# Kernel optimization log

Hardware: AMD Instinct MI355X
Metric: run time of the kernel (lower is better)

Reference implementation:

```python
import jax, jax.numpy as jnp
import numpy as np

NC = 80            # num_classes
REG_MAX = 16
STRIDES = (8, 16, 32)
IMG = 640.0
TOPK = 10
TAL_ALPHA = 0.5
TAL_BETA = 6.0
L_BOX, L_CLS, L_DFL = 7.5, 0.5, 1.5
EPS = 1e-9
NEG = -1e8


def bbox_iou(b1, b2, ciou=False, eps=1e-7):
    # b1, b2: (..., 4) xyxy, broadcastable
    inter_wh = jnp.clip(jnp.minimum(b1[..., 2:], b2[..., 2:]) - jnp.maximum(b1[..., :2], b2[..., :2]), 0.0)
    inter = inter_wh[..., 0] * inter_wh[..., 1]
    w1 = jnp.clip(b1[..., 2] - b1[..., 0], 0.0); h1 = jnp.clip(b1[..., 3] - b1[..., 1], 0.0)
    w2 = jnp.clip(b2[..., 2] - b2[..., 0], 0.0); h2 = jnp.clip(b2[..., 3] - b2[..., 1], 0.0)
    union = w1 * h1 + w2 * h2 - inter + eps
    iou = inter / union
    if not ciou:
        return iou
    cx1 = (b1[..., 0] + b1[..., 2]) * 0.5; cy1 = (b1[..., 1] + b1[..., 3]) * 0.5
    cx2 = (b2[..., 0] + b2[..., 2]) * 0.5; cy2 = (b2[..., 1] + b2[..., 3]) * 0.5
    rho2 = (cx2 - cx1) ** 2 + (cy2 - cy1) ** 2
    cw = jnp.maximum(b1[..., 2], b2[..., 2]) - jnp.minimum(b1[..., 0], b2[..., 0])
    ch = jnp.maximum(b1[..., 3], b2[..., 3]) - jnp.minimum(b1[..., 1], b2[..., 1])
    c2 = cw ** 2 + ch ** 2 + eps
    v = (4.0 / np.pi ** 2) * (jnp.arctan(w2 / (h2 + eps)) - jnp.arctan(w1 / (h1 + eps))) ** 2
    alpha = jax.lax.stop_gradient(v / (1.0 - iou + v + eps))  # torch computes alpha under no_grad
    return iou - (rho2 / c2 + alpha * v)


def _assign_one(pred_scores, pred_bboxes, anchor_points, gt_labels, gt_bboxes):
    """TaskAlignedAssigner for one image.
    pred_scores (N,nc), pred_bboxes (N,4), anchor_points (N,2), gt_labels (M,), gt_bboxes (M,4).
    Returns target_bboxes (N,4), target_scores (N,nc), fg_mask (N,)."""
    N = pred_bboxes.shape[0]; M = gt_bboxes.shape[0]
    gl = jnp.clip(gt_labels.astype(jnp.int32), 0, NC - 1)
    x = anchor_points[:, 0]; y = anchor_points[:, 1]
    l = x[:, None] - gt_bboxes[None, :, 0]
    t = y[:, None] - gt_bboxes[None, :, 1]
    r = gt_bboxes[None, :, 2] - x[:, None]
    b = gt_bboxes[None, :, 3] - y[:, None]
    in_gts = (l > 0) & (t > 0) & (r > 0) & (b > 0)                     # (N,M)
    ious = bbox_iou(pred_bboxes[:, None, :], gt_bboxes[None, :, :])    # (N,M)
    cls_score = pred_scores[:, gl]                                     # (N,M)
    align = jnp.clip(cls_score, 0.0) ** TAL_ALPHA * jnp.clip(ious, 0.0) ** TAL_BETA
    align = jnp.where(in_gts, align, NEG)
    k = min(TOPK, N)
    _, topk_idx = jax.lax.top_k(align.T, k)                            # (M,k) indices into N
    mask_topk = jnp.zeros((M, N), dtype=bool).at[jnp.arange(M)[:, None], topk_idx].set(True).T
    mask_pos = mask_topk & in_gts                                      # (N,M)
    ious_pos = jnp.where(mask_pos, ious, -1.0)
    max_iou = ious_pos.max(axis=1)
    gt_idx = ious_pos.argmax(axis=1)                                   # (N,)
    fg_mask = max_iou > -0.5
    metric_pos = jnp.where(mask_pos, align, NEG)
    metric_max = jnp.clip(metric_pos.max(axis=0), EPS)                 # (M,)
    rows = jnp.arange(N)
    score = align[rows, gt_idx] / metric_max[gt_idx] * ious[rows, gt_idx]
    score = jnp.clip(score, 0.0, 1.0) * fg_mask.astype(pred_scores.dtype)
    tcls = gl[gt_idx]
    target_scores = jnp.zeros((N, NC), dtype=pred_scores.dtype).at[rows, tcls].set(score)
    target_bboxes = jnp.where(fg_mask[:, None], gt_bboxes[gt_idx], 0.0)
    return target_bboxes, target_scores, fg_mask


def _df_loss(reg_logits, target):
    # reg_logits (B,N,4,R) logits, target (B,N,4) float in [0,R-1] -> (B,N)
    t = jnp.clip(target, 0.0, float(REG_MAX - 1))
    left = jnp.floor(t).astype(jnp.int32)
    right = jnp.minimum(left + 1, REG_MAX - 1)
    wl = right.astype(t.dtype) - t
    wr = t - left.astype(t.dtype)
    same = right == left
    wl = jnp.where(same, 1.0, wl)
    wr = jnp.where(same, 0.0, wr)
    logp = jax.nn.log_softmax(reg_logits, axis=-1)
    ll = -jnp.take_along_axis(logp, left[..., None], axis=-1)[..., 0]
    lr = -jnp.take_along_axis(logp, right[..., None], axis=-1)[..., 0]
    return (ll * wl + lr * wr).sum(axis=-1)


def _forward(p0, p1, p2, gt_bboxes, gt_labels):
    preds = [p0, p1, p2]
    B = p0.shape[0]
    reg_ch = 4 * REG_MAX
    cls_list, reg_list, ap_list, st_list = [], [], [], []
    for p, s in zip(preds, STRIDES):
        _, _, h, w = p.shape
        reg = p[:, :reg_ch]
        cls = p[:, reg_ch:]
        cls_list.append(cls.transpose(0, 2, 3, 1).reshape(B, -1, NC))
        reg_list.append(reg.transpose(0, 2, 3, 1).reshape(B, -1, 4, REG_MAX))
        gy, gx = jnp.meshgrid(jnp.arange(h), jnp.arange(w), indexing='ij')
        pts = jnp.stack([(gx + 0.5) * s, (gy + 0.5) * s], axis=-1).reshape(-1, 2).astype(p.dtype)
        ap_list.append(pts)
        st_list.append(jnp.full((h * w,), float(s), dtype=p.dtype))
    cls_logits = jnp.concatenate(cls_list, axis=1)      # (B,N,nc)
    reg_logits = jnp.concatenate(reg_list, axis=1)      # (B,N,4,R)
    anchor_points = jnp.concatenate(ap_list, axis=0)    # (N,2)
    stride_t = jnp.concatenate(st_list, axis=0)         # (N,)
    pred_scores = jax.nn.sigmoid(cls_logits)
    proj = jnp.arange(REG_MAX, dtype=cls_logits.dtype)
    dist = (jax.nn.softmax(reg_logits, axis=-1) * proj).sum(-1) * stride_t[None, :, None]  # (B,N,4)
    ax = anchor_points[:, 0]; ay = anchor_points[:, 1]
    pred_bboxes = jnp.stack([ax - dist[..., 0], ay - dist[..., 1], ax + dist[..., 2], ay + dist[..., 3]], axis=-1)
    # --- TAL assignment (runs under no_grad in torch) ---
    tb, ts, fg = jax.vmap(lambda ps, pb, gl, gb: _assign_one(ps, pb, anchor_points, gl, gb))(
        jax.lax.stop_gradient(pred_scores), jax.lax.stop_gradient(pred_bboxes), gt_labels, gt_bboxes)
    tb = jax.lax.stop_gradient(tb)
    ts = jax.lax.stop_gradient(ts)
    ts_sum = jnp.maximum(ts.sum(), 1.0)
    # --- cls: BCE with logits over all anchors/classes ---
    z = cls_logits
    bce = jnp.clip(z, 0.0) - z * ts + jnp.log1p(jnp.exp(-jnp.abs(z)))
    loss_cls = bce.sum() / ts_sum
    # --- box: CIoU weighted by target score, fg only ---
    weight = ts.sum(-1) * fg.astype(ts.dtype)           # (B,N)
    ciou = bbox_iou(pred_bboxes, tb, ciou=True)         # (B,N)
    loss_box = ((1.0 - ciou) * weight).sum() / ts_sum
    # --- dfl ---
    inv_s = 1.0 / stride_t
    tl = (ax - tb[..., 0]) * inv_s
    tt = (ay - tb[..., 1]) * inv_s
    tr = (tb[..., 2] - ax) * inv_s
    tbm = (tb[..., 3] - ay) * inv_s
    target_ltrb = jnp.clip(jnp.stack([tl, tt, tr, tbm], axis=-1), 0.0, float(REG_MAX - 1))
    dfl = _df_loss(reg_logits, target_ltrb)             # (B,N)
    loss_dfl = (dfl * weight).sum() / ts_sum
    return L_BOX * loss_box + L_CLS * loss_cls + L_DFL * loss_dfl


def setup_inputs() -> dict:
    key = jax.random.key(0)
    k0, k1, k2, kc, kw, kl = jax.random.split(key, 6)
    B, C = 16, 4 * REG_MAX + NC
    p0 = jax.random.normal(k0, (B, C, 80, 80), dtype=jnp.float32)
    p1 = jax.random.normal(k1, (B, C, 40, 40), dtype=jnp.float32)
    p2 = jax.random.normal(k2, (B, C, 20, 20), dtype=jnp.float32)
    M = 32
    cxy = jax.random.uniform(kc, (B, M, 2), minval=64.0, maxval=IMG - 64.0)
    wh = jax.random.uniform(kw, (B, M, 2), minval=16.0, maxval=128.0)
    gt_bboxes = jnp.concatenate([cxy - wh * 0.5, cxy + wh * 0.5], axis=-1).astype(jnp.float32)
    gt_labels = jax.random.randint(kl, (B, M), 0, NC, dtype=jnp.int32).astype(jnp.int64)
    return {"p0": p0, "p1": p1, "p2": p2, "gt_bboxes": gt_bboxes, "gt_labels": gt_labels}


def reference(p0, p1, p2, gt_bboxes, gt_labels):
    return _forward(p0, p1, p2, gt_bboxes, gt_labels)
```

## Files before the change

### kernel.cpp

```cpp
#include <hip/hip_runtime.h>

#define BATCH 16
#define NANCH 8400
#define MGT 32
#define NCLS 80
#define RCH 64
#define NCH 144
#define TOPKK 10
#define MAXC 576
#define PBLK 2100
#define TKB 512
#define BCEB 2625
#define FINB 525

struct AInfo { int lvl, pos, W, HW; float s, ax, ay; };

__device__ __forceinline__ AInfo anchor_of(int n) {
  AInfo a;
  if (n < 6400)      { a.lvl = 0; a.pos = n;        a.W = 80; a.HW = 6400; a.s = 8.f;  }
  else if (n < 8000) { a.lvl = 1; a.pos = n - 6400; a.W = 40; a.HW = 1600; a.s = 16.f; }
  else               { a.lvl = 2; a.pos = n - 8000; a.W = 20; a.HW = 400;  a.s = 32.f; }
  int px = a.pos % a.W, py = a.pos / a.W;
  a.ax = (px + 0.5f) * a.s;
  a.ay = (py + 0.5f) * a.s;
  return a;
}

__device__ __forceinline__ const float* lvl_ptr(const float* p0, const float* p1,
                                                const float* p2, int lvl) {
  return lvl == 0 ? p0 : (lvl == 1 ? p1 : p2);
}

__device__ __forceinline__ float iou_xyxy(float4 a, float4 b) {
  float ix = fmaxf(fminf(a.z, b.z) - fmaxf(a.x, b.x), 0.f);
  float iy = fmaxf(fminf(a.w, b.w) - fmaxf(a.y, b.y), 0.f);
  float inter = ix * iy;
  float w1 = fmaxf(a.z - a.x, 0.f), h1 = fmaxf(a.w - a.y, 0.f);
  float w2 = fmaxf(b.z - b.x, 0.f), h2 = fmaxf(b.w - b.y, 0.f);
  float uni = w1 * h1 + w2 * h2 - inter + 1e-7f;
  return inter / uni;
}

__device__ __forceinline__ float ciou_xyxy(float4 a, float4 b) {
  const float eps = 1e-7f;
  float ix = fmaxf(fminf(a.z, b.z) - fmaxf(a.x, b.x), 0.f);
  float iy = fmaxf(fminf(a.w, b.w) - fmaxf(a.y, b.y), 0.f);
  float inter = ix * iy;
  float w1 = fmaxf(a.z - a.x, 0.f), h1 = fmaxf(a.w - a.y, 0.f);
  float w2 = fmaxf(b.z - b.x, 0.f), h2 = fmaxf(b.w - b.y, 0.f);
  float uni = w1 * h1 + w2 * h2 - inter + eps;
  float iou = inter / uni;
  float cx1 = (a.x + a.z) * 0.5f, cy1 = (a.y + a.w) * 0.5f;
  float cx2 = (b.x + b.z) * 0.5f, cy2 = (b.y + b.w) * 0.5f;
  float rho2 = (cx2 - cx1) * (cx2 - cx1) + (cy2 - cy1) * (cy2 - cy1);
  float cw = fmaxf(a.z, b.z) - fminf(a.x, b.x);
  float ch = fmaxf(a.w, b.w) - fminf(a.y, b.y);
  float c2 = cw * cw + ch * ch + eps;
  const float kpi = 4.f / (float)(M_PI * M_PI);
  float dat = atanf(w2 / (h2 + eps)) - atanf(w1 / (h1 + eps));
  float v = kpi * dat * dat;
  float alpha = v / (1.f - iou + v + eps);
  return iou - (rho2 / c2 + alpha * v);
}

__device__ __forceinline__ float block_sum256(float v) {
  __shared__ float sm[4];
  #pragma unroll
  for (int off = 32; off; off >>= 1) v += __shfl_xor(v, off);
  __syncthreads();
  if ((threadIdx.x & 63) == 0) sm[threadIdx.x >> 6] = v;
  __syncthreads();
  return (threadIdx.x == 0) ? (sm[0] + sm[1] + sm[2] + sm[3]) : 0.f;
}

__global__ __launch_bounds__(256) void k_pre(
    const float* __restrict__ p0, const float* __restrict__ p1, const float* __restrict__ p2,
    float* __restrict__ pboxf, float* __restrict__ logz,
    unsigned long long* __restrict__ slots, double* __restrict__ accum) {
  int blk = blockIdx.x, tid = threadIdx.x;
  if (blk == 0 && tid < 8) accum[tid] = 0.0;
  int q = blk & 3;
  int i = (blk >> 2) * 256 + tid;
  int b = i / NANCH, n = i % NANCH;
  AInfo A = anchor_of(n);
  const float* p = lvl_ptr(p0, p1, p2, A.lvl);
  size_t base = (size_t)b * NCH * A.HW + A.pos;

  float z[16]; float zm = -1e30f;
  #pragma unroll
  for (int j = 0; j < 16; ++j) {
    z[j] = p[base + (size_t)(q * 16 + j) * A.HW];
    zm = fmaxf(zm, z[j]);
  }
  float se = 0.f, ae = 0.f;
  #pragma unroll
  for (int j = 0; j < 16; ++j) {
    float e = __expf(z[j] - zm);
    se += e; ae += e * (float)j;
  }
  float d = ae / se * A.s;
  float val = (q == 0) ? A.ax - d : (q == 1) ? A.ay - d : (q == 2) ? A.ax + d : A.ay + d;
  pboxf[(size_t)i * 4 + q] = val;
  logz[(size_t)i * 4 + q] = zm + __logf(se);
  if (q == 0) slots[i] = 0ULL;
}

__global__ __launch_bounds__(256) void k_mid(
    const float* __restrict__ p0, const float* __restrict__ p1, const float* __restrict__ p2,
    const float4* __restrict__ pbox, const float* __restrict__ gtb, const int* __restrict__ gtl,
    float* __restrict__ metric_max, unsigned long long* __restrict__ slots,
    float* __restrict__ bce_part) {
  __shared__ float val[MAXC];
  __shared__ int   idx[MAXC];
  __shared__ float cio[MAXC];
  __shared__ float rv[4];
  __shared__ int   ri[4], rs[4], sdone[1];
  int blk = blockIdx.x, tid = threadIdx.x;

  if (blk >= TKB) {
    int r = blk - TKB;
    int i = r * 256 + tid;
    float lb = 0.f;
    #pragma unroll
    for (int j = 0; j < 4; ++j) {
      int u = i + j * 672000;
      int b = u / 168000;
      int rr = u % 168000;
      const float4* src;
      if (rr < 128000)      src = (const float4*)p0 + ((size_t)(b * NCH + RCH) * 1600 + rr);
      else if (rr < 160000) src = (const float4*)p1 + ((size_t)(b * NCH + RCH) * 400 + (rr - 128000));
      else                  src = (const float4*)p2 + ((size_t)(b * NCH + RCH) * 100 + (rr - 160000));
      float4 z4 = *src;
      lb += fmaxf(z4.x, 0.f) + __logf(1.f + __expf(-fabsf(z4.x)));
      lb += fmaxf(z4.y, 0.f) + __logf(1.f + __expf(-fabsf(z4.y)));
      lb += fmaxf(z4.z, 0.f) + __logf(1.f + __expf(-fabsf(z4.z)));
      lb += fmaxf(z4.w, 0.f) + __logf(1.f + __expf(-fabsf(z4.w)));
    }
    float tot = block_sum256(lb);
    if (tid == 0) bce_part[r] = tot;
    return;
  }

  int b = blk >> 5, m = blk & 31;
  float4 g = ((const float4*)gtb)[b * MGT + m];
  int gl = min(max(gtl[b * MGT + m], 0), NCLS - 1);

  const int   Ws[3] = {80, 40, 20};
  const float ss[3] = {8.f, 16.f, 32.f};
  const int   nb[3] = {0, 6400, 8000};
  int x0[3], y0[3], nxl[3], cb[3];
  int cnt = 0;
  #pragma unroll
  for (int L = 0; L < 3; ++L) {
    float s = ss[L]; int W = Ws[L];
    int ax0 = max((int)floorf(g.x / s - 0.5f), 0);
    int ax1 = min((int)ceilf (g.z / s - 0.5f), W - 1);
    int ay0 = max((int)floorf(g.y / s - 0.5f), 0);
    int ay1 = min((int)ceilf (g.w / s - 0.5f), W - 1);
    int nx = max(ax1 - ax0 + 1, 0);
    int ny = max(ay1 - ay0 + 1, 0);
    x0[L] = ax0; y0[L] = ay0; nxl[L] = nx;
    cb[L] = cnt; cnt += nx * ny;
  }
  int C = min(cnt, MAXC);

  for (int t = tid; t < C; t += 256) {
    int L = (t >= cb[2]) ? 2 : (t >= cb[1]) ? 1 : 0;
    int r = t - cb[L];
    int ix = r % nxl[L], iy = r / nxl[L];
    int px = x0[L] + ix, py = y0[L] + iy;
    float ax = (px + 0.5f) * ss[L], ay = (py + 0.5f) * ss[L];
    float al = -3e38f, iou = 0.f; int n = 0x7fffffff;
    if (ax > g.x && ay > g.y && ax < g.z && ay < g.w) {
      n = nb[L] + py * Ws[L] + px;
      iou = iou_xyxy(pbox[(size_t)b * NANCH + n], g);
      int HW = (L == 0) ? 6400 : (L == 1) ? 1600 : 400;
      const float* p = lvl_ptr(p0, p1, p2, L);
      float z = p[(size_t)b * NCH * HW + (size_t)(RCH + gl) * HW + (py * Ws[L] + px)];
      float sg = 1.f / (1.f + __expf(-z));
      float i3 = iou * iou * iou;
      al = sqrtf(sg) * i3 * i3;
    }
    val[t] = al; idx[t] = n; cio[t] = iou;
  }
  __syncthreads();

  float mmax = -1.f;
  for (int k = 0; k < TOPKK; ++k) {
    float bv = -3e38f; int bn = 0x7fffffff, bs = 0;
    for (int t = tid; t < C; t += 256) {
      float v = val[t]; int n2 = idx[t];
      if (v > bv || (v == bv && n2 < bn)) { bv = v; bn = n2; bs = t; }
    }
    #pragma unroll
    for (int off = 32; off; off >>= 1) {
      float ov = __shfl_xor(bv, off);
      int   on = __shfl_xor(bn, off);
      int   os = __shfl_xor(bs, off);
      if (ov > bv || (ov == bv && on < bn)) { bv = ov; bn = on; bs = os; }
    }
    if ((tid & 63) == 0) { rv[tid >> 6] = bv; ri[tid >> 6] = bn; rs[tid >> 6] = bs; }
    __syncthreads();
    if (tid == 0) {
      #pragma unroll
      for (int w = 1; w < 4; ++w)
        if (rv[w] > bv || (rv[w] == bv && ri[w] < bn)) { bv = rv[w]; bn = ri[w]; bs = rs[w]; }
      if (bv >= 0.f) {
        mmax = fmaxf(mmax, bv);
        unsigned long long key = (1ULL << 62) |
                                 ((unsigned long long)__float_as_uint(cio[bs]) << 6) |
                                 (unsigned long long)(31 - m);
        atomicMax(&slots[(size_t)b * NANCH + bn], key);
        val[bs] = -3e38f;
        sdone[0] = 0;
      } else sdone[0] = 1;
    }
    __syncthreads();
    if (sdone[0]) break;
  }
  if (tid == 0) metric_max[b * MGT + m] = fmaxf(mmax, 1e-9f);
}

__global__ __launch_bounds__(256) void k_final(
    const float* __restrict__ p0, const float* __restrict__ p1, const float* __restrict__ p2,
    const float4* __restrict__ pbox, const float* __restrict__ logz,
    const float* __restrict__ gtb, const int* __restrict__ gtl,
    const float* __restrict__ metric_max, const unsigned long long* __restrict__ slots,
    double* __restrict__ accum) {
  int i = blockIdx.x * 256 + threadIdx.x;
  unsigned long long key = slots[i];
  float ts_p = 0.f, zc_p = 0.f, box_p = 0.f, dfl_p = 0.f;
  if (key) {
    int b = i / NANCH, n = i % NANCH;
    int m = 31 - (int)(key & 63ULL);
    float iou = __uint_as_float((unsigned int)((key >> 6) & 0xFFFFFFFFULL));
    AInfo A = anchor_of(n);
    float4 g = ((const float4*)gtb)[b * MGT + m];
    int gl = min(max(gtl[b * MGT + m], 0), NCLS - 1);
    const float* p = lvl_ptr(p0, p1, p2, A.lvl);
    size_t base = (size_t)b * NCH * A.HW + A.pos;

    float z = p[base + (size_t)(RCH + gl) * A.HW];
    float sg = 1.f / (1.f + __expf(-z));
    float i3 = iou * iou * iou;
    float align = sqrtf(sg) * i3 * i3;
    float mm = metric_max[b * MGT + m];
    float score = fminf(fmaxf(align / mm * iou, 0.f), 1.f);

    ts_p = score;
    zc_p = z * score;

    float4 pb = pbox[i];
    float ciou = ciou_xyxy(pb, g);
    box_p = (1.f - ciou) * score;

    float4 lz4 = ((const float4*)logz)[i];
    float inv_s = 1.f / A.s;
    float targ0 = (A.ax - g.x) * inv_s;
    float targ1 = (A.ay - g.y) * inv_s;
    float targ2 = (g.z - A.ax) * inv_s;
    float targ3 = (g.w - A.ay) * inv_s;
    float dfl = 0.f;
    #pragma unroll
    for (int sd = 0; sd < 4; ++sd) {
      float tg = sd == 0 ? targ0 : sd == 1 ? targ1 : sd == 2 ? targ2 : targ3;
      float lZ = sd == 0 ? lz4.x : sd == 1 ? lz4.y : sd == 2 ? lz4.z : lz4.w;
      float t = fminf(fmaxf(tg, 0.f), 15.f);
      int left = (int)floorf(t);
      int right = min(left + 1, 15);
      float wl, wr;
      if (right == left) { wl = 1.f; wr = 0.f; }
      else               { wl = (float)right - t; wr = t - (float)left; }
      float zl = p[base + (size_t)(sd * 16 + left)  * A.HW];
      float zr = p[base + (size_t)(sd * 16 + right) * A.HW];
      dfl += wl * (lZ - zl) + wr * (lZ - zr);
    }
    dfl_p = dfl * score;
  }
  float s;
  s = block_sum256(ts_p);  if (threadIdx.x == 0 && s != 0.f) atomicAdd(&accum[4], (double)s);
  s = block_sum256(zc_p);  if (threadIdx.x == 0 && s != 0.f) atomicAdd(&accum[1], (double)s);
  s = block_sum256(box_p); if (threadIdx.x == 0 && s != 0.f) atomicAdd(&accum[2], (double)s);
  s = block_sum256(dfl_p); if (threadIdx.x == 0 && s != 0.f) atomicAdd(&accum[3], (double)s);
}

__global__ void k_out(const double* __restrict__ accum, const float* __restrict__ bce_part,
                      float* __restrict__ out) {
  int tid = threadIdx.x;
  float s = 0.f;
  for (int t = tid; t < BCEB; t += 256) s += bce_part[t];
  s = block_sum256(s);
  if (tid == 0) {
    double ts = fmax(accum[4], 1.0);
    double loss = 7.5 * accum[2] / ts +
                  0.5 * ((double)s - accum[1]) / ts +
                  1.5 * accum[3] / ts;
    out[0] = (float)loss;
  }
}

extern "C" void kernel_launch(void* const* d_in, const int* in_sizes, int n_in,
                              void* d_out, int out_size, void* d_ws, size_t ws_size,
                              hipStream_t stream) {
  const float* p0  = (const float*)d_in[0];
  const float* p1  = (const float*)d_in[1];
  const float* p2  = (const float*)d_in[2];
  const float* gtb = (const float*)d_in[3];
  const int*   gtl = (const int*)d_in[4];
  float* out = (float*)d_out;

  char* ws = (char*)d_ws;
  double* accum      = (double*)ws;
  float*  metric_max = (float*)(ws + 64);
  float*  bce_part   = (float*)(ws + 2112);
  float*  pboxf      = (float*)(ws + 12624);
  float4* pbox       = (float4*)(ws + 12624);
  float*  logz       = (float*)(ws + 2163024);
  unsigned long long* slots = (unsigned long long*)(ws + 4313424);

  k_pre<<<PBLK, 256, 0, stream>>>(p0, p1, p2, pboxf, logz, slots, accum);
  k_mid<<<TKB + BCEB, 256, 0, stream>>>(p0, p1, p2, pbox, gtb, gtl, metric_max, slots, bce_part);
  k_final<<<FINB, 256, 0, stream>>>(p0, p1, p2, pbox, logz, gtb, gtl,
                                    metric_max, slots, accum);
  k_out<<<1, 256, 0, stream>>>(accum, bce_part, out);
}
```

Measured before the change: 147.0 us.

## Merge decode and top-k kernels, recompute candidate boxes, drop atomics

Folds the box-decode pre-pass into the top-k/BCE kernel as an extra block range, so one launch covers all three jobs. Top-k blocks now decode their candidate anchor boxes inline from the raw logits instead of reading the precomputed pbox. Slots are zeroed with a memset, and the final kernel writes per-block partial sums that the output kernel reduces in double, replacing double atomics. This removes a launch and the serialization between decode and top-k, at the cost of redundant DFL softmax work for overlapping candidates.

```diff
diff --git a/kernel.cpp b/kernel.cpp
--- a/kernel.cpp
+++ b/kernel.cpp
@@ -8,9 +8,10 @@
 #define NCH 144
 #define TOPKK 10
 #define MAXC 576
-#define PBLK 2100
 #define TKB 512
+#define DECB 2100
 #define BCEB 2625
+#define TOTB (TKB + DECB + BCEB)
 #define FINB 525
 
 struct AInfo { int lvl, pos, W, HW; float s, ax, ay; };
@@ -29,6 +30,28 @@
 __device__ __forceinline__ const float* lvl_ptr(const float* p0, const float* p1,
                                                 const float* p2, int lvl) {
   return lvl == 0 ? p0 : (lvl == 1 ? p1 : p2);
+}
+
+__device__ __forceinline__ float4 decode_box(const float* __restrict__ p, size_t chbase,
+                                             int HW, float s, float ax, float ay) {
+  float d[4];
+  #pragma unroll
+  for (int q = 0; q < 4; ++q) {
+    float z[16]; float zm = -1e30f;
+    #pragma unroll
+    for (int j = 0; j < 16; ++j) {
+      z[j] = p[chbase + (size_t)(q * 16 + j) * HW];
+      zm = fmaxf(zm, z[j]);
+    }
+    float se = 0.f, ae = 0.f;
+    #pragma unroll
+    for (int j = 0; j < 16; ++j) {
+      float e = __expf(z[j] - zm);
+      se += e; ae += e * (float)j;
+    }
+    d[q] = ae / se * s;
+  }
+  return make_float4(ax - d[0], ay - d[1], ax + d[2], ay + d[3]);
 }
 
 __device__ __forceinline__ float iou_xyxy(float4 a, float4 b) {
@@ -73,41 +96,20 @@
   return (threadIdx.x == 0) ? (sm[0] + sm[1] + sm[2] + sm[3]) : 0.f;
 }
 
-__global__ __launch_bounds__(256) void k_pre(
+__device__ __forceinline__ double block_sum256d(double v) {
+  __shared__ double smd[4];
+  #pragma unroll
+  for (int off = 32; off; off >>= 1) v += __shfl_xor(v, off);
+  __syncthreads();
+  if ((threadIdx.x & 63) == 0) smd[threadIdx.x >> 6] = v;
+  __syncthreads();
+  return (threadIdx.x == 0) ? (smd[0] + smd[1] + smd[2] + smd[3]) : 0.0;
+}
+
+__global__ __launch_bounds__(256) void k_one(
     const float* __restrict__ p0, const float* __restrict__ p1, const float* __restrict__ p2,
+    const float* __restrict__ gtb, const int* __restrict__ gtl,
     float* __restrict__ pboxf, float* __restrict__ logz,
-    unsigned long long* __restrict__ slots, double* __restrict__ accum) {
-  int blk = blockIdx.x, tid = threadIdx.x;
-  if (blk == 0 && tid < 8) accum[tid] = 0.0;
-  int q = blk & 3;
-  int i = (blk >> 2) * 256 + tid;
-  int b = i / NANCH, n = i % NANCH;
-  AInfo A = anchor_of(n);
-  const float* p = lvl_ptr(p0, p1, p2, A.lvl);
-  size_t base = (size_t)b * NCH * A.HW + A.pos;
-
-  float z[16]; float zm = -1e30f;
-  #pragma unroll
-  for (int j = 0; j < 16; ++j) {
-    z[j] = p[base + (size_t)(q * 16 + j) * A.HW];
-    zm = fmaxf(zm, z[j]);
-  }
-  float se = 0.f, ae = 0.f;
-  #pragma unroll
-  for (int j = 0; j < 16; ++j) {
-    float e = __expf(z[j] - zm);
-    se += e; ae += e * (float)j;
-  }
-  float d = ae / se * A.s;
-  float val = (q == 0) ? A.ax - d : (q == 1) ? A.ay - d : (q == 2) ? A.ax + d : A.ay + d;
-  pboxf[(size_t)i * 4 + q] = val;
-  logz[(size_t)i * 4 + q] = zm + __logf(se);
-  if (q == 0) slots[i] = 0ULL;
-}
-
-__global__ __launch_bounds__(256) void k_mid(
-    const float* __restrict__ p0, const float* __restrict__ p1, const float* __restrict__ p2,
-    const float4* __restrict__ pbox, const float* __restrict__ gtb, const int* __restrict__ gtl,
     float* __restrict__ metric_max, unsigned long long* __restrict__ slots,
     float* __restrict__ bce_part) {
   __shared__ float val[MAXC];
@@ -117,8 +119,8 @@
   __shared__ int   ri[4], rs[4], sdone[1];
   int blk = blockIdx.x, tid = threadIdx.x;
 
-  if (blk >= TKB) {
-    int r = blk - TKB;
+  if (blk >= TKB + DECB) {
+    int r = blk - (TKB + DECB);
     int i = r * 256 + tid;
     float lb = 0.f;
     #pragma unroll
@@ -138,6 +140,34 @@
     }
     float tot = block_sum256(lb);
     if (tid == 0) bce_part[r] = tot;
+    return;
+  }
+
+  if (blk >= TKB) {
+    int db = blk - TKB;
+    int q = db & 3;
+    int i = (db >> 2) * 256 + tid;
+    int b = i / NANCH, n = i % NANCH;
+    AInfo A = anchor_of(n);
+    const float* p = lvl_ptr(p0, p1, p2, A.lvl);
+    size_t base = (size_t)b * NCH * A.HW + A.pos;
+
+    float z[16]; float zm = -1e30f;
+    #pragma unroll
+    for (int j = 0; j < 16; ++j) {
+      z[j] = p[base + (size_t)(q * 16 + j) * A.HW];
+      zm = fmaxf(zm, z[j]);
+    }
+    float se = 0.f, ae = 0.f;
+    #pragma unroll
+    for (int j = 0; j < 16; ++j) {
+      float e = __expf(z[j] - zm);
+      se += e; ae += e * (float)j;
+    }
+    float d = ae / se * A.s;
+    float v = (q == 0) ? A.ax - d : (q == 1) ? A.ay - d : (q == 2) ? A.ax + d : A.ay + d;
+    pboxf[(size_t)i * 4 + q] = v;
+    logz[(size_t)i * 4 + q] = zm + __logf(se);
     return;
   }
 
@@ -172,11 +202,15 @@
     float ax = (px + 0.5f) * ss[L], ay = (py + 0.5f) * ss[L];
     float al = -3e38f, iou = 0.f; int n = 0x7fffffff;
     if (ax > g.x && ay > g.y && ax < g.z && ay < g.w) {
-      n = nb[L] + py * Ws[L] + px;
-      iou = iou_xyxy(pbox[(size_t)b * NANCH + n], g);
+      int W = Ws[L];
       int HW = (L == 0) ? 6400 : (L == 1) ? 1600 : 400;
+      int pos = py * W + px;
+      n = nb[L] + pos;
       const float* p = lvl_ptr(p0, p1, p2, L);
-      float z = p[(size_t)b * NCH * HW + (size_t)(RCH + gl) * HW + (py * Ws[L] + px)];
+      size_t chbase = (size_t)b * NCH * HW + pos;
+      float4 pb = decode_box(p, chbase, HW, ss[L], ax, ay);
+      iou = iou_xyxy(pb, g);
+      float z = p[chbase + (size_t)(RCH + gl) * HW];
       float sg = 1.f / (1.f + __expf(-z));
       float i3 = iou * iou * iou;
       al = sqrtf(sg) * i3 * i3;
@@ -221,12 +255,12 @@
   if (tid == 0) metric_max[b * MGT + m] = fmaxf(mmax, 1e-9f);
 }
 
-__global__ __launch_bounds__(256) void k_final(
+__global__ __launch_bounds__(256) void k_fin(
     const float* __restrict__ p0, const float* __restrict__ p1, const float* __restrict__ p2,
     const float4* __restrict__ pbox, const float* __restrict__ logz,
     const float* __restrict__ gtb, const int* __restrict__ gtl,
     const float* __restrict__ metric_max, const unsigned long long* __restrict__ slots,
-    double* __restrict__ accum) {
+    float4* __restrict__ fin_part) {
   int i = blockIdx.x * 256 + threadIdx.x;
   unsigned long long key = slots[i];
   float ts_p = 0.f, zc_p = 0.f, box_p = 0.f, dfl_p = 0.f;
@@ -277,25 +311,30 @@
     }
     dfl_p = dfl * score;
   }
-  float s;
-  s = block_sum256(ts_p);  if (threadIdx.x == 0 && s != 0.f) atomicAdd(&accum[4], (double)s);
-  s = block_sum256(zc_p);  if (threadIdx.x == 0 && s != 0.f) atomicAdd(&accum[1], (double)s);
-  s = block_sum256(box_p); if (threadIdx.x == 0 && s != 0.f) atomicAdd(&accum[2], (double)s);
-  s = block_sum256(dfl_p); if (threadIdx.x == 0 && s != 0.f) atomicAdd(&accum[3], (double)s);
-}
-
-__global__ void k_out(const double* __restrict__ accum, const float* __restrict__ bce_part,
+  float s0 = block_sum256(box_p);
+  float s1 = block_sum256(zc_p);
+  float s2 = block_sum256(dfl_p);
+  float s3 = block_sum256(ts_p);
+  if (threadIdx.x == 0) fin_part[blockIdx.x] = make_float4(s0, s1, s2, s3);
+}
+
+__global__ void k_out(const float* __restrict__ bce_part, const float4* __restrict__ fin_part,
                       float* __restrict__ out) {
   int tid = threadIdx.x;
-  float s = 0.f;
-  for (int t = tid; t < BCEB; t += 256) s += bce_part[t];
-  s = block_sum256(s);
+  double sb = 0.0, s0 = 0.0, s1 = 0.0, s2 = 0.0, s3 = 0.0;
+  for (int t = tid; t < BCEB; t += 256) sb += (double)bce_part[t];
+  for (int t = tid; t < FINB; t += 256) {
+    float4 f = fin_part[t];
+    s0 += (double)f.x; s1 += (double)f.y; s2 += (double)f.z; s3 += (double)f.w;
+  }
+  sb = block_sum256d(sb);
+  s0 = block_sum256d(s0);
+  s1 = block_sum256d(s1);
+  s2 = block_sum256d(s2);
+  s3 = block_sum256d(s3);
   if (tid == 0) {
-    double ts = fmax(accum[4], 1.0);
-    double loss = 7.5 * accum[2] / ts +
-                  0.5 * ((double)s - accum[1]) / ts +
-                  1.5 * accum[3] / ts;
-    out[0] = (float)loss;
+    double ts = fmax(s3, 1.0);
+    out[0] = (float)(7.5 * s0 / ts + 0.5 * (sb - s1) / ts + 1.5 * s2 / ts);
   }
 }
 
@@ -310,17 +349,18 @@
   float* out = (float*)d_out;
 
   char* ws = (char*)d_ws;
-  double* accum      = (double*)ws;
-  float*  metric_max = (float*)(ws + 64);
-  float*  bce_part   = (float*)(ws + 2112);
-  float*  pboxf      = (float*)(ws + 12624);
-  float4* pbox       = (float4*)(ws + 12624);
-  float*  logz       = (float*)(ws + 2163024);
-  unsigned long long* slots = (unsigned long long*)(ws + 4313424);
-
-  k_pre<<<PBLK, 256, 0, stream>>>(p0, p1, p2, pboxf, logz, slots, accum);
-  k_mid<<<TKB + BCEB, 256, 0, stream>>>(p0, p1, p2, pbox, gtb, gtl, metric_max, slots, bce_part);
-  k_final<<<FINB, 256, 0, stream>>>(p0, p1, p2, pbox, logz, gtb, gtl,
-                                    metric_max, slots, accum);
-  k_out<<<1, 256, 0, stream>>>(accum, bce_part, out);
-}
+  float*  metric_max = (float*)ws;
+  float*  bce_part   = (float*)(ws + 2048);
+  float4* fin_part   = (float4*)(ws + 12560);
+  float*  pboxf      = (float*)(ws + 20960);
+  float4* pbox       = (float4*)(ws + 20960);
+  float*  logz       = (float*)(ws + 2171360);
+  unsigned long long* slots = (unsigned long long*)(ws + 4321760);
+
+  hipMemsetAsync(slots, 0, (size_t)BATCH * NANCH * 8, stream);
+  k_one<<<TOTB, 256, 0, stream>>>(p0, p1, p2, gtb, gtl, pboxf, logz,
+                                  metric_max, slots, bce_part);
+  k_fin<<<FINB, 256, 0, stream>>>(p0, p1, p2, pbox, logz, gtb, gtl,
+                                  metric_max, slots, fin_part);
+  k_out<<<1, 256, 0, stream>>>(bce_part, fin_part, out);
+}
```

Result: faster. 135.3 us (-7.9%).
